# Performance work log

Measured on AMD Instinct MI355X. Metric: run time of the kernel, lower is better.

Reference implementation:

```python
import jax, jax.numpy as jnp
import numpy as np

NUM_HEADS = 16
HEAD_SIZE = 64
D_MODEL = NUM_HEADS * HEAD_SIZE  # 1024


def setup_inputs() -> dict:
    key = jax.random.key(0)
    ks = jax.random.split(key, 12)
    B, S = 4, 2048
    q = jax.random.normal(ks[0], (B, S, D_MODEL), dtype=jnp.float32)
    k = jax.random.normal(ks[1], (B, S, D_MODEL), dtype=jnp.float32)
    v = jax.random.normal(ks[2], (B, S, D_MODEL), dtype=jnp.float32)
    w = jax.random.uniform(ks[3], (B, S), dtype=jnp.float32)
    scale = 1.0 / np.sqrt(D_MODEL)
    Wq = jax.random.normal(ks[4], (D_MODEL, D_MODEL), dtype=jnp.float32) * scale
    Wk = jax.random.normal(ks[5], (D_MODEL, D_MODEL), dtype=jnp.float32) * scale
    Wv = jax.random.normal(ks[6], (D_MODEL, D_MODEL), dtype=jnp.float32) * scale
    Wo = jax.random.normal(ks[7], (D_MODEL, D_MODEL), dtype=jnp.float32) * scale
    bq = jnp.zeros((D_MODEL,), jnp.float32)
    bk = jnp.zeros((D_MODEL,), jnp.float32)
    bv = jnp.zeros((D_MODEL,), jnp.float32)
    bo = jnp.zeros((D_MODEL,), jnp.float32)
    return {"q": q, "k": k, "v": v, "w": w,
            "Wq": Wq, "bq": bq, "Wk": Wk, "bk": bk,
            "Wv": Wv, "bv": bv, "Wo": Wo, "bo": bo}


def reference(q, k, v, w, Wq, bq, Wk, bk, Wv, bv, Wo, bo):
    B, S, _ = q.shape
    H, Dh = NUM_HEADS, HEAD_SIZE

    def split_heads(x):  # [B,S,D] -> [B,H,S,Dh]
        return x.reshape(B, -1, H, Dh).transpose(0, 2, 1, 3)

    q_h = split_heads(q @ Wq + bq)
    k_h = split_heads(k @ Wk + bk)
    v_h = split_heads(v @ Wv + bv)

    # [B,H,Sq,Sk]
    score = jnp.einsum('bhqd,bhkd->bhqk', q_h, k_h) / jnp.sqrt(
        jnp.asarray(Dh, jnp.float32))
    # weighted unnormalized softmax: exp(score)*w / sum (no max subtraction,
    # faithful to original)
    exp_score = jnp.exp(score) * w[:, None, None, :]
    attn = exp_score / (jnp.sum(exp_score, axis=-1, keepdims=True) + 1e-12)

    context = jnp.einsum('bhqk,bhkd->bhqd', attn, v_h)  # [B,H,S,Dh]
    context = context.transpose(0, 2, 1, 3).reshape(B, -1, H * Dh)
    return context @ Wo + bo
```

## Files before the change

### kernel.cpp

```cpp
#include <hip/hip_runtime.h>
#include <hip/hip_bf16.h>

typedef __bf16 bf16x8 __attribute__((ext_vector_type(8)));
typedef float f32x4 __attribute__((ext_vector_type(4)));
typedef float f32x16 __attribute__((ext_vector_type(16)));
typedef unsigned short u16;
typedef unsigned int u32;

#define SB 4
#define SS 2048
#define SD 1024
#define SH 16
#define SDH 64

__device__ __forceinline__ u16 f2bf(float f) {
  union { float f; u32 u; } x; x.f = f;
  u32 r = (x.u + 0x7FFFu + ((x.u >> 16) & 1u)) >> 16;
  return (u16)r;
}

__device__ __forceinline__ void gl_lds16(const void* g, void* l) {
  __builtin_amdgcn_global_load_lds(
      (__attribute__((address_space(1))) void*)g,
      (__attribute__((address_space(3))) void*)l, 16, 0, 0);
}

__global__ void cast_bf16_kernel(const float* __restrict__ in,
                                 u32* __restrict__ out, int n8) {
  int i = blockIdx.x * blockDim.x + threadIdx.x;
  if (i >= n8) return;
  const float4* inp = (const float4*)in;
  float4 a = inp[2 * i], b = inp[2 * i + 1];
  uint4 o;
  o.x = (u32)f2bf(a.x) | ((u32)f2bf(a.y) << 16);
  o.y = (u32)f2bf(a.z) | ((u32)f2bf(a.w) << 16);
  o.z = (u32)f2bf(b.x) | ((u32)f2bf(b.y) << 16);
  o.w = (u32)f2bf(b.z) | ((u32)f2bf(b.w) << 16);
  ((uint4*)out)[i] = o;
}

__global__ void transpose_cast_kernel(const float* __restrict__ W,
                                      u16* __restrict__ Wt) {
  __shared__ float t[32][33];
  int bx = blockIdx.x, by = blockIdx.y;
  int tx = threadIdx.x, ty = threadIdx.y;
#pragma unroll
  for (int j = 0; j < 32; j += 8)
    t[ty + j][tx] = W[(size_t)(by * 32 + ty + j) * SD + bx * 32 + tx];
  __syncthreads();
#pragma unroll
  for (int j = 0; j < 32; j += 8)
    Wt[(size_t)(bx * 32 + ty + j) * SD + by * 32 + tx] = f2bf(t[tx][ty + j]);
}

template <int MODE>
__global__ __launch_bounds__(256, 2)
void gemm_bt(const u16* __restrict__ A, const u16* __restrict__ Bt,
             const float* __restrict__ bias, void* __restrict__ Out,
             int M, int N, int K) {
  __shared__ u16 Asl[128 * 32];
  __shared__ u16 Bsl[128 * 32];
  const int ntile = N >> 7;
  int bid = blockIdx.x;
  bid = (bid & 7) * ((int)gridDim.x >> 3) + (bid >> 3);
  int m0 = (bid / ntile) * 128, n0 = (bid % ntile) * 128;
  int tid = threadIdx.x;
  int lane = tid & 63, wv = tid >> 6;
  int wr = wv >> 1, wc = wv & 1;

  f32x4 acc[4][4] = {};

  for (int k0 = 0; k0 < K; k0 += 32) {
#pragma unroll
    for (int it = 0; it < 2; ++it) {
      int c = tid + it * 256;
      int row = c >> 2, sl = c & 3;
      gl_lds16(A + (size_t)(m0 + row) * K + k0 + sl * 8, (char*)Asl + c * 16);
      gl_lds16(Bt + (size_t)(n0 + row) * K + k0 + sl * 8, (char*)Bsl + c * 16);
    }
    __syncthreads();
    bf16x8 af[4], bfr[4];
#pragma unroll
    for (int i = 0; i < 4; ++i) {
      int ar = wr * 64 + i * 16 + (lane & 15);
      af[i] = *(const bf16x8*)&Asl[ar * 32 + (lane >> 4) * 8];
      int br = wc * 64 + i * 16 + (lane & 15);
      bfr[i] = *(const bf16x8*)&Bsl[br * 32 + (lane >> 4) * 8];
    }
#pragma unroll
    for (int i = 0; i < 4; ++i)
#pragma unroll
      for (int j = 0; j < 4; ++j)
        acc[i][j] = __builtin_amdgcn_mfma_f32_16x16x32_bf16(af[i], bfr[j],
                                                            acc[i][j], 0, 0, 0);
    __syncthreads();
  }

  int cg = lane >> 4, cc = lane & 15;
#pragma unroll
  for (int i = 0; i < 4; ++i) {
#pragma unroll
    for (int j = 0; j < 4; ++j) {
#pragma unroll
      for (int r = 0; r < 4; ++r) {
        int m = m0 + wr * 64 + i * 16 + cg * 4 + r;
        int n = n0 + wc * 64 + j * 16 + cc;
        float val = acc[i][j][r];
        if (MODE == 0) {
          val = (val + bias[n]) * 0.125f;
          int b = m >> 11, s = m & 2047, h = n >> 6, dh = n & 63;
          ((u16*)Out)[((size_t)((b * SH + h) * SS + s) << 6) + dh] = f2bf(val);
        } else if (MODE == 1) {
          val += bias[n];
          int b = m >> 11, s = m & 2047, h = n >> 6, dh = n & 63;
          ((u16*)Out)[((size_t)((b * SH + h) * SS + s) << 6) + dh] = f2bf(val);
        } else if (MODE == 2) {
          val += bias[m];
          int h = m >> 6, dh = m & 63, b = n >> 11, s = n & 2047;
          ((u16*)Out)[((size_t)((b * SH + h) * SDH + dh) << 11) + s] = f2bf(val);
        } else {
          val += bias[n];
          ((float*)Out)[(size_t)m * N + n] = val;
        }
      }
    }
  }
}

__global__ __launch_bounds__(256, 3)
void attn_kernel(const u16* __restrict__ Qh, const u16* __restrict__ Kh,
                 const u16* __restrict__ Vt, const float* __restrict__ w,
                 u16* __restrict__ Ctx) {
  __shared__ u16 Kl[2][4096];
  __shared__ u16 Vl[2][4096];
  __shared__ float wl[SS];

  int bid = blockIdx.x;
  int swz = (bid & 7) * 128 + (bid >> 3);
  int bh = swz >> 4;
  int qt = swz & 15;
  int b = bh >> 4, hh = bh & 15;
  int q0 = qt * 128;
  int tid = threadIdx.x, lane = tid & 63, wv = tid >> 6;
  int ql = lane & 31, h = lane >> 5;
  const size_t basebh = (size_t)bh * (SS * SDH);

  auto stage = [&](int buf, int t) {
    int kv0 = t * 64;
#pragma unroll
    for (int it = 0; it < 2; ++it) {
      int c = tid + it * 256;
      int row = c >> 3, sl = c & 7;
      int ssl = sl ^ (row & 7);
      gl_lds16(Kh + basebh + (size_t)(kv0 + row) * SDH + ssl * 8,
               (char*)&Kl[buf][0] + c * 16);
      gl_lds16(Vt + basebh + (size_t)row * SS + kv0 + ssl * 8,
               (char*)&Vl[buf][0] + c * 16);
    }
  };

  stage(0, 0);

  const float* wb = w + b * SS;
  for (int i = tid; i < SS; i += 256) wl[i] = __logf(wb[i]);

  bf16x8 qf[4];
  {
    const u16* qp = Qh + basebh + (size_t)(q0 + wv * 32 + ql) * SDH + h * 8;
#pragma unroll
    for (int st = 0; st < 4; ++st) qf[st] = *(const bf16x8*)(qp + st * 16);
  }

  f32x16 ctx0 = {}, ctx1 = {};
  float rs = 0.f;
  u32 pk[8][2];

  auto process = [&](const u16* Kb, const u16* Vb, int kv0) {
#pragma unroll
    for (int kt = 0; kt < 2; ++kt) {
      f32x16 sc = {};
      __builtin_amdgcn_s_setprio(1);
#pragma unroll
      for (int st = 0; st < 4; ++st) {
        int krow = kt * 32 + ql;
        int byt = (krow * 128 + (st * 16 + h * 8) * 2) ^ ((krow & 7) << 4);
        bf16x8 kf = *(const bf16x8*)((const char*)Kb + byt);
        sc = __builtin_amdgcn_mfma_f32_32x32x16_bf16(kf, qf[st], sc, 0, 0, 0);
      }
      __builtin_amdgcn_s_setprio(0);
#pragma unroll
      for (int e2 = 0; e2 < 4; ++e2) {
        float4 lw = *(const float4*)&wl[kv0 + kt * 32 + e2 * 8 + h * 4];
        float v0 = __expf(sc[e2 * 4 + 0] + lw.x);
        float v1 = __expf(sc[e2 * 4 + 1] + lw.y);
        float v2 = __expf(sc[e2 * 4 + 2] + lw.z);
        float v3 = __expf(sc[e2 * 4 + 3] + lw.w);
        rs += (v0 + v1) + (v2 + v3);
        u32 p0, p1;
        asm("v_cvt_pk_bf16_f32 %0, %1, %2" : "=v"(p0) : "v"(v0), "v"(v1));
        asm("v_cvt_pk_bf16_f32 %0, %1, %2" : "=v"(p1) : "v"(v2), "v"(v3));
        pk[kt * 4 + e2][0] = p0;
        pk[kt * 4 + e2][1] = p1;
      }
    }
#pragma unroll
    for (int ksl = 0; ksl < 4; ++ksl) {
      u32 d0 = pk[2 * ksl][0], d1 = pk[2 * ksl][1];
      u32 s0 = pk[2 * ksl + 1][0], s1 = pk[2 * ksl + 1][1];
      asm("v_permlane32_swap_b32 %0, %1" : "+v"(d0), "+v"(s0));
      asm("v_permlane32_swap_b32 %0, %1" : "+v"(d1), "+v"(s1));
      union { u32 u[4]; bf16x8 v; } pa;
      pa.u[0] = d0; pa.u[1] = d1; pa.u[2] = s0; pa.u[3] = s1;
      __builtin_amdgcn_s_setprio(1);
      {
        int byt0 = (ql * 128 + (ksl * 16 + h * 8) * 2) ^ ((ql & 7) << 4);
        bf16x8 vf0 = *(const bf16x8*)((const char*)Vb + byt0);
        ctx0 = __builtin_amdgcn_mfma_f32_32x32x16_bf16(pa.v, vf0, ctx0, 0, 0, 0);
        int vr1 = 32 + ql;
        int byt1 = (vr1 * 128 + (ksl * 16 + h * 8) * 2) ^ ((vr1 & 7) << 4);
        bf16x8 vf1 = *(const bf16x8*)((const char*)Vb + byt1);
        ctx1 = __builtin_amdgcn_mfma_f32_32x32x16_bf16(pa.v, vf1, ctx1, 0, 0, 0);
      }
      __builtin_amdgcn_s_setprio(0);
    }
  };

  for (int t = 0; t < 32; t += 2) {
    asm volatile("s_waitcnt vmcnt(0)" ::: "memory");
    __syncthreads();
    if (t + 1 < 32) stage(1, t + 1);
    process(&Kl[0][0], &Vl[0][0], t * 64);
    asm volatile("s_waitcnt vmcnt(0)" ::: "memory");
    __syncthreads();
    if (t + 2 < 32) stage(0, t + 2);
    process(&Kl[1][0], &Vl[1][0], (t + 1) * 64);
  }

  rs += __shfl_xor(rs, 32, 64);
  float rinv = 1.0f / (rs + 1e-12f);

#pragma unroll
  for (int reg = 0; reg < 16; ++reg) {
    int qrow = (reg & 3) + 8 * (reg >> 2) + 4 * h;
    float ri = __shfl(rinv, qrow, 64);
    int srow = q0 + wv * 32 + qrow;
    size_t base = ((size_t)(b * SS + srow) << 10) + hh * SDH;
    Ctx[base + ql] = f2bf(ctx0[reg] * ri);
    Ctx[base + 32 + ql] = f2bf(ctx1[reg] * ri);
  }
}

extern "C" void kernel_launch(void* const* d_in, const int* in_sizes, int n_in,
                              void* d_out, int out_size, void* d_ws,
                              size_t ws_size, hipStream_t stream) {
  const float* q = (const float*)d_in[0];
  const float* k = (const float*)d_in[1];
  const float* v = (const float*)d_in[2];
  const float* w = (const float*)d_in[3];
  const float* Wq = (const float*)d_in[4];
  const float* bq = (const float*)d_in[5];
  const float* Wk = (const float*)d_in[6];
  const float* bk = (const float*)d_in[7];
  const float* Wv = (const float*)d_in[8];
  const float* bv = (const float*)d_in[9];
  const float* Wo = (const float*)d_in[10];
  const float* bo = (const float*)d_in[11];
  float* out = (float*)d_out;

  char* ws = (char*)d_ws;
  const size_t SZ = (size_t)8192 * 1024 * 2;
  u16* qb = (u16*)(ws);
  u16* kb = (u16*)(ws + SZ);
  u16* vb = (u16*)(ws + 2 * SZ);
  u16* WqT = (u16*)(ws + 3 * SZ);
  u16* WkT = WqT + 1024 * 1024;
  u16* WvT = WkT + 1024 * 1024;
  u16* WoT = WvT + 1024 * 1024;
  u16* Qh = (u16*)(ws + 3 * SZ + (size_t)4 * 1024 * 1024 * 2);
  u16* Kh = Qh + (size_t)8192 * 1024;
  u16* Vt = Kh + (size_t)8192 * 1024;
  u16* Ctx = qb;

  cast_bf16_kernel<<<4096, 256, 0, stream>>>(q, (u32*)qb, 1048576);
  cast_bf16_kernel<<<4096, 256, 0, stream>>>(k, (u32*)kb, 1048576);
  cast_bf16_kernel<<<4096, 256, 0, stream>>>(v, (u32*)vb, 1048576);

  dim3 tb(32, 8), tg(32, 32);
  transpose_cast_kernel<<<tg, tb, 0, stream>>>(Wq, WqT);
  transpose_cast_kernel<<<tg, tb, 0, stream>>>(Wk, WkT);
  transpose_cast_kernel<<<tg, tb, 0, stream>>>(Wv, WvT);
  transpose_cast_kernel<<<tg, tb, 0, stream>>>(Wo, WoT);

  gemm_bt<0><<<512, 256, 0, stream>>>(qb, WqT, bq, Qh, 8192, 1024, 1024);
  gemm_bt<1><<<512, 256, 0, stream>>>(kb, WkT, bk, Kh, 8192, 1024, 1024);
  gemm_bt<2><<<512, 256, 0, stream>>>(WvT, vb, bv, Vt, 1024, 8192, 1024);

  attn_kernel<<<1024, 256, 0, stream>>>(Qh, Kh, Vt, w, Ctx);

  gemm_bt<3><<<512, 256, 0, stream>>>(Ctx, WoT, bo, out, 8192, 1024, 1024);
}
```

Baseline: 254.4 us.

## Double-buffer GEMM with K=64 swizzled tiles and enlarge attention tiles with exp2

The projection GEMM now uses double-buffered LDS tiles of depth 64 with an XOR swizzle, prefetching the next tile while computing the current one. The attention kernel processes 256 queries per block (two 32-row groups per wave) over 128-key stages, so each K/V tile loaded into LDS is reused by twice as many queries. The log-weight is preloaded as the MFMA accumulator init, and exp is replaced with exp2 by folding log2(e) into the Q scale; log weights use a native log. The cost is larger LDS use, lower occupancy (launch bounds 2), half as many attention blocks, and a base-2 log/exp mismatch unless w's log is also base 2.

```diff
diff --git a/kernel.cpp b/kernel.cpp
--- a/kernel.cpp
+++ b/kernel.cpp
@@ -58,8 +58,8 @@
 void gemm_bt(const u16* __restrict__ A, const u16* __restrict__ Bt,
              const float* __restrict__ bias, void* __restrict__ Out,
              int M, int N, int K) {
-  __shared__ u16 Asl[128 * 32];
-  __shared__ u16 Bsl[128 * 32];
+  __shared__ u16 Asl[2][128 * 64];
+  __shared__ u16 Bsl[2][128 * 64];
   const int ntile = N >> 7;
   int bid = blockIdx.x;
   bid = (bid & 7) * ((int)gridDim.x >> 3) + (bid >> 3);
@@ -68,31 +68,50 @@
   int lane = tid & 63, wv = tid >> 6;
   int wr = wv >> 1, wc = wv & 1;
 
+  auto stage = [&](int buf, int k0) {
+#pragma unroll
+    for (int it = 0; it < 4; ++it) {
+      int c = tid + it * 256;
+      int row = c >> 3, sl = c & 7;
+      int ssl = sl ^ (row & 7);
+      gl_lds16(A + (size_t)(m0 + row) * K + k0 + ssl * 8,
+               (char*)&Asl[buf][0] + c * 16);
+      gl_lds16(Bt + (size_t)(n0 + row) * K + k0 + ssl * 8,
+               (char*)&Bsl[buf][0] + c * 16);
+    }
+  };
+
   f32x4 acc[4][4] = {};
-
-  for (int k0 = 0; k0 < K; k0 += 32) {
-#pragma unroll
-    for (int it = 0; it < 2; ++it) {
-      int c = tid + it * 256;
-      int row = c >> 2, sl = c & 3;
-      gl_lds16(A + (size_t)(m0 + row) * K + k0 + sl * 8, (char*)Asl + c * 16);
-      gl_lds16(Bt + (size_t)(n0 + row) * K + k0 + sl * 8, (char*)Bsl + c * 16);
-    }
-    __syncthreads();
-    bf16x8 af[4], bfr[4];
-#pragma unroll
-    for (int i = 0; i < 4; ++i) {
-      int ar = wr * 64 + i * 16 + (lane & 15);
-      af[i] = *(const bf16x8*)&Asl[ar * 32 + (lane >> 4) * 8];
-      int br = wc * 64 + i * 16 + (lane & 15);
-      bfr[i] = *(const bf16x8*)&Bsl[br * 32 + (lane >> 4) * 8];
-    }
-#pragma unroll
-    for (int i = 0; i < 4; ++i)
-#pragma unroll
-      for (int j = 0; j < 4; ++j)
-        acc[i][j] = __builtin_amdgcn_mfma_f32_16x16x32_bf16(af[i], bfr[j],
-                                                            acc[i][j], 0, 0, 0);
+  stage(0, 0);
+  asm volatile("s_waitcnt vmcnt(0)" ::: "memory");
+  __syncthreads();
+
+  int nk = K >> 6;
+  for (int kt = 0; kt < nk; ++kt) {
+    int buf = kt & 1;
+    if (kt + 1 < nk) stage(buf ^ 1, (kt + 1) << 6);
+#pragma unroll
+    for (int kk = 0; kk < 2; ++kk) {
+      bf16x8 af[4], bfr[4];
+#pragma unroll
+      for (int i = 0; i < 4; ++i) {
+        int ar = wr * 64 + i * 16 + (lane & 15);
+        int abyt = (ar * 128 + (kk * 32 + (lane >> 4) * 8) * 2) ^
+                   ((ar & 7) << 4);
+        af[i] = *(const bf16x8*)((const char*)&Asl[buf][0] + abyt);
+        int br = wc * 64 + i * 16 + (lane & 15);
+        int bbyt = (br * 128 + (kk * 32 + (lane >> 4) * 8) * 2) ^
+                   ((br & 7) << 4);
+        bfr[i] = *(const bf16x8*)((const char*)&Bsl[buf][0] + bbyt);
+      }
+#pragma unroll
+      for (int i = 0; i < 4; ++i)
+#pragma unroll
+        for (int j = 0; j < 4; ++j)
+          acc[i][j] = __builtin_amdgcn_mfma_f32_16x16x32_bf16(
+              af[i], bfr[j], acc[i][j], 0, 0, 0);
+    }
+    asm volatile("s_waitcnt vmcnt(0)" ::: "memory");
     __syncthreads();
   }
 
@@ -107,7 +126,7 @@
         int n = n0 + wc * 64 + j * 16 + cc;
         float val = acc[i][j][r];
         if (MODE == 0) {
-          val = (val + bias[n]) * 0.125f;
+          val = (val + bias[n]) * 0.18033688011112042f;
           int b = m >> 11, s = m & 2047, h = n >> 6, dh = n & 63;
           ((u16*)Out)[((size_t)((b * SH + h) * SS + s) << 6) + dh] = f2bf(val);
         } else if (MODE == 1) {
@@ -127,34 +146,34 @@
   }
 }
 
-__global__ __launch_bounds__(256, 3)
+__global__ __launch_bounds__(256, 2)
 void attn_kernel(const u16* __restrict__ Qh, const u16* __restrict__ Kh,
                  const u16* __restrict__ Vt, const float* __restrict__ w,
                  u16* __restrict__ Ctx) {
-  __shared__ u16 Kl[2][4096];
-  __shared__ u16 Vl[2][4096];
+  __shared__ u16 Kl[2][8192];
+  __shared__ u16 Vl[2][8192];
   __shared__ float wl[SS];
 
   int bid = blockIdx.x;
-  int swz = (bid & 7) * 128 + (bid >> 3);
-  int bh = swz >> 4;
-  int qt = swz & 15;
+  int swz = (bid & 7) * 64 + (bid >> 3);
+  int bh = swz >> 3;
+  int qt = swz & 7;
   int b = bh >> 4, hh = bh & 15;
-  int q0 = qt * 128;
+  int q0 = qt * 256;
   int tid = threadIdx.x, lane = tid & 63, wv = tid >> 6;
   int ql = lane & 31, h = lane >> 5;
   const size_t basebh = (size_t)bh * (SS * SDH);
 
   auto stage = [&](int buf, int t) {
-    int kv0 = t * 64;
-#pragma unroll
-    for (int it = 0; it < 2; ++it) {
+    int kv0 = t * 128;
+#pragma unroll
+    for (int it = 0; it < 4; ++it) {
       int c = tid + it * 256;
-      int row = c >> 3, sl = c & 7;
-      int ssl = sl ^ (row & 7);
-      gl_lds16(Kh + basebh + (size_t)(kv0 + row) * SDH + ssl * 8,
+      int kr = c >> 3, ks = c & 7;
+      gl_lds16(Kh + basebh + (size_t)(kv0 + kr) * SDH + (ks ^ (kr & 7)) * 8,
                (char*)&Kl[buf][0] + c * 16);
-      gl_lds16(Vt + basebh + (size_t)row * SS + kv0 + ssl * 8,
+      int vr = c >> 4, vs = c & 15;
+      gl_lds16(Vt + basebh + (size_t)vr * SS + kv0 + (vs ^ (vr & 7)) * 8,
                (char*)&Vl[buf][0] + c * 16);
     }
   };
@@ -162,91 +181,121 @@
   stage(0, 0);
 
   const float* wb = w + b * SS;
-  for (int i = tid; i < SS; i += 256) wl[i] = __logf(wb[i]);
-
-  bf16x8 qf[4];
-  {
-    const u16* qp = Qh + basebh + (size_t)(q0 + wv * 32 + ql) * SDH + h * 8;
-#pragma unroll
-    for (int st = 0; st < 4; ++st) qf[st] = *(const bf16x8*)(qp + st * 16);
-  }
-
-  f32x16 ctx0 = {}, ctx1 = {};
-  float rs = 0.f;
-  u32 pk[8][2];
-
-  auto process = [&](const u16* Kb, const u16* Vb, int kv0) {
-#pragma unroll
-    for (int kt = 0; kt < 2; ++kt) {
-      f32x16 sc = {};
-      __builtin_amdgcn_s_setprio(1);
-#pragma unroll
-      for (int st = 0; st < 4; ++st) {
-        int krow = kt * 32 + ql;
-        int byt = (krow * 128 + (st * 16 + h * 8) * 2) ^ ((krow & 7) << 4);
-        bf16x8 kf = *(const bf16x8*)((const char*)Kb + byt);
-        sc = __builtin_amdgcn_mfma_f32_32x32x16_bf16(kf, qf[st], sc, 0, 0, 0);
+  for (int i = tid; i < SS; i += 256)
+    wl[i] = __builtin_amdgcn_logf(wb[i]);
+
+  bf16x8 qf[2][4];
+#pragma unroll
+  for (int u = 0; u < 2; ++u) {
+    const u16* qp =
+        Qh + basebh + (size_t)(q0 + wv * 64 + u * 32 + ql) * SDH + h * 8;
+#pragma unroll
+    for (int st = 0; st < 4; ++st) qf[u][st] = *(const bf16x8*)(qp + st * 16);
+  }
+
+  f32x16 ctx[2][2] = {};
+  float rs[2] = {0.f, 0.f};
+
+  asm volatile("s_waitcnt vmcnt(0)" ::: "memory");
+  __syncthreads();
+
+  for (int t = 0; t < 16; ++t) {
+    int buf = t & 1;
+    if (t + 1 < 16) stage(buf ^ 1, t + 1);
+#pragma unroll
+    for (int half = 0; half < 2; ++half) {
+      const char* Kb = (const char*)&Kl[buf][half * 4096];
+      const char* Vb = (const char*)&Vl[buf][0];
+      int vc0 = half * 64;
+      int kvb = t * 128 + half * 64;
+      u32 pk[2][8][2];
+#pragma unroll
+      for (int kt = 0; kt < 2; ++kt) {
+        bf16x8 kf[4];
+#pragma unroll
+        for (int st = 0; st < 4; ++st) {
+          int krow = kt * 32 + ql;
+          int byt = (krow * 128 + (st * 16 + h * 8) * 2) ^ ((krow & 7) << 4);
+          kf[st] = *(const bf16x8*)(Kb + byt);
+        }
+        float4 lw[4];
+#pragma unroll
+        for (int e2 = 0; e2 < 4; ++e2)
+          lw[e2] = *(const float4*)&wl[kvb + kt * 32 + e2 * 8 + h * 4];
+#pragma unroll
+        for (int u = 0; u < 2; ++u) {
+          f32x16 sc;
+#pragma unroll
+          for (int e2 = 0; e2 < 4; ++e2) {
+            sc[e2 * 4 + 0] = lw[e2].x;
+            sc[e2 * 4 + 1] = lw[e2].y;
+            sc[e2 * 4 + 2] = lw[e2].z;
+            sc[e2 * 4 + 3] = lw[e2].w;
+          }
+          __builtin_amdgcn_s_setprio(1);
+#pragma unroll
+          for (int st = 0; st < 4; ++st)
+            sc = __builtin_amdgcn_mfma_f32_32x32x16_bf16(kf[st], qf[u][st],
+                                                         sc, 0, 0, 0);
+          __builtin_amdgcn_s_setprio(0);
+#pragma unroll
+          for (int e2 = 0; e2 < 4; ++e2) {
+            float v0 = __builtin_amdgcn_exp2f(sc[e2 * 4 + 0]);
+            float v1 = __builtin_amdgcn_exp2f(sc[e2 * 4 + 1]);
+            float v2 = __builtin_amdgcn_exp2f(sc[e2 * 4 + 2]);
+            float v3 = __builtin_amdgcn_exp2f(sc[e2 * 4 + 3]);
+            rs[u] += (v0 + v1) + (v2 + v3);
+            u32 p0, p1;
+            asm("v_cvt_pk_bf16_f32 %0, %1, %2" : "=v"(p0) : "v"(v0), "v"(v1));
+            asm("v_cvt_pk_bf16_f32 %0, %1, %2" : "=v"(p1) : "v"(v2), "v"(v3));
+            pk[u][kt * 4 + e2][0] = p0;
+            pk[u][kt * 4 + e2][1] = p1;
+          }
+        }
       }
-      __builtin_amdgcn_s_setprio(0);
-#pragma unroll
-      for (int e2 = 0; e2 < 4; ++e2) {
-        float4 lw = *(const float4*)&wl[kv0 + kt * 32 + e2 * 8 + h * 4];
-        float v0 = __expf(sc[e2 * 4 + 0] + lw.x);
-        float v1 = __expf(sc[e2 * 4 + 1] + lw.y);
-        float v2 = __expf(sc[e2 * 4 + 2] + lw.z);
-        float v3 = __expf(sc[e2 * 4 + 3] + lw.w);
-        rs += (v0 + v1) + (v2 + v3);
-        u32 p0, p1;
-        asm("v_cvt_pk_bf16_f32 %0, %1, %2" : "=v"(p0) : "v"(v0), "v"(v1));
-        asm("v_cvt_pk_bf16_f32 %0, %1, %2" : "=v"(p1) : "v"(v2), "v"(v3));
-        pk[kt * 4 + e2][0] = p0;
-        pk[kt * 4 + e2][1] = p1;
+#pragma unroll
+      for (int ksl = 0; ksl < 4; ++ksl) {
+        int cb = (vc0 + ksl * 16 + h * 8) * 2;
+        int byt0 = (ql * 256 + cb) ^ ((ql & 7) << 4);
+        bf16x8 vf0 = *(const bf16x8*)(Vb + byt0);
+        int vr1 = 32 + ql;
+        int byt1 = (vr1 * 256 + cb) ^ ((vr1 & 7) << 4);
+        bf16x8 vf1 = *(const bf16x8*)(Vb + byt1);
+#pragma unroll
+        for (int u = 0; u < 2; ++u) {
+          u32 d0 = pk[u][2 * ksl][0], d1 = pk[u][2 * ksl][1];
+          u32 s0 = pk[u][2 * ksl + 1][0], s1 = pk[u][2 * ksl + 1][1];
+          asm("v_permlane32_swap_b32 %0, %1" : "+v"(d0), "+v"(s0));
+          asm("v_permlane32_swap_b32 %0, %1" : "+v"(d1), "+v"(s1));
+          union { u32 uu[4]; bf16x8 v; } pa;
+          pa.uu[0] = d0; pa.uu[1] = d1; pa.uu[2] = s0; pa.uu[3] = s1;
+          __builtin_amdgcn_s_setprio(1);
+          ctx[u][0] = __builtin_amdgcn_mfma_f32_32x32x16_bf16(
+              pa.v, vf0, ctx[u][0], 0, 0, 0);
+          ctx[u][1] = __builtin_amdgcn_mfma_f32_32x32x16_bf16(
+              pa.v, vf1, ctx[u][1], 0, 0, 0);
+          __builtin_amdgcn_s_setprio(0);
+        }
       }
     }
-#pragma unroll
-    for (int ksl = 0; ksl < 4; ++ksl) {
-      u32 d0 = pk[2 * ksl][0], d1 = pk[2 * ksl][1];
-      u32 s0 = pk[2 * ksl + 1][0], s1 = pk[2 * ksl + 1][1];
-      asm("v_permlane32_swap_b32 %0, %1" : "+v"(d0), "+v"(s0));
-      asm("v_permlane32_swap_b32 %0, %1" : "+v"(d1), "+v"(s1));
-      union { u32 u[4]; bf16x8 v; } pa;
-      pa.u[0] = d0; pa.u[1] = d1; pa.u[2] = s0; pa.u[3] = s1;
-      __builtin_amdgcn_s_setprio(1);
-      {
-        int byt0 = (ql * 128 + (ksl * 16 + h * 8) * 2) ^ ((ql & 7) << 4);
-        bf16x8 vf0 = *(const bf16x8*)((const char*)Vb + byt0);
-        ctx0 = __builtin_amdgcn_mfma_f32_32x32x16_bf16(pa.v, vf0, ctx0, 0, 0, 0);
-        int vr1 = 32 + ql;
-        int byt1 = (vr1 * 128 + (ksl * 16 + h * 8) * 2) ^ ((vr1 & 7) << 4);
-        bf16x8 vf1 = *(const bf16x8*)((const char*)Vb + byt1);
-        ctx1 = __builtin_amdgcn_mfma_f32_32x32x16_bf16(pa.v, vf1, ctx1, 0, 0, 0);
-      }
-      __builtin_amdgcn_s_setprio(0);
-    }
-  };
-
-  for (int t = 0; t < 32; t += 2) {
     asm volatile("s_waitcnt vmcnt(0)" ::: "memory");
     __syncthreads();
-    if (t + 1 < 32) stage(1, t + 1);
-    process(&Kl[0][0], &Vl[0][0], t * 64);
-    asm volatile("s_waitcnt vmcnt(0)" ::: "memory");
-    __syncthreads();
-    if (t + 2 < 32) stage(0, t + 2);
-    process(&Kl[1][0], &Vl[1][0], (t + 1) * 64);
-  }
-
-  rs += __shfl_xor(rs, 32, 64);
-  float rinv = 1.0f / (rs + 1e-12f);
-
-#pragma unroll
-  for (int reg = 0; reg < 16; ++reg) {
-    int qrow = (reg & 3) + 8 * (reg >> 2) + 4 * h;
-    float ri = __shfl(rinv, qrow, 64);
-    int srow = q0 + wv * 32 + qrow;
-    size_t base = ((size_t)(b * SS + srow) << 10) + hh * SDH;
-    Ctx[base + ql] = f2bf(ctx0[reg] * ri);
-    Ctx[base + 32 + ql] = f2bf(ctx1[reg] * ri);
+  }
+
+#pragma unroll
+  for (int u = 0; u < 2; ++u) {
+    float rsu = rs[u];
+    rsu += __shfl_xor(rsu, 32, 64);
+    float rinv = 1.0f / (rsu + 1e-12f);
+#pragma unroll
+    for (int reg = 0; reg < 16; ++reg) {
+      int qrow = (reg & 3) + 8 * (reg >> 2) + 4 * h;
+      float ri = __shfl(rinv, qrow, 64);
+      int srow = q0 + wv * 64 + u * 32 + qrow;
+      size_t base = ((size_t)(b * SS + srow) << 10) + hh * SDH;
+      Ctx[base + ql] = f2bf(ctx[u][0][reg] * ri);
+      Ctx[base + 32 + ql] = f2bf(ctx[u][1][reg] * ri);
+    }
   }
 }
 
@@ -295,7 +344,7 @@
   gemm_bt<1><<<512, 256, 0, stream>>>(kb, WkT, bk, Kh, 8192, 1024, 1024);
   gemm_bt<2><<<512, 256, 0, stream>>>(WvT, vb, bv, Vt, 1024, 8192, 1024);
 
-  attn_kernel<<<1024, 256, 0, stream>>>(Qh, Kh, Vt, w, Ctx);
+  attn_kernel<<<512, 256, 0, stream>>>(Qh, Kh, Vt, w, Ctx);
 
   gemm_bt<3><<<512, 256, 0, stream>>>(Ctx, WoT, bo, out, 8192, 1024, 1024);
 }
```

After: 215.5 us. -15.3%, faster.
